# Kernel optimization log

Hardware: AMD Instinct MI355X
Metric: run time of the kernel (lower is better)

The kernel has to match this reference:

```python
import jax, jax.numpy as jnp
import numpy as np

TAU_MIN = 0.1
TAU_MAX = 5.0
EPS = 1e-8


def setup_inputs() -> dict:
    key = jax.random.key(0)
    ks = jax.random.split(key, 5)
    B, DK, NK, DV, H = 16384, 512, 4096, 512, 32
    return {
        "q": jax.random.normal(ks[0], (B, DK), dtype=jnp.float32),
        "keys": jax.random.normal(ks[1], (NK, DK), dtype=jnp.float32),
        "values": jax.random.normal(ks[2], (NK, DV), dtype=jnp.float32),
        "w1": jax.random.normal(ks[3], (H, 1), dtype=jnp.float32) * (6.0 / (H + 1)) ** 0.5,
        "b1": jnp.zeros((H,), dtype=jnp.float32),
        "w2": jax.random.normal(ks[4], (1, H), dtype=jnp.float32) * (6.0 / (H + 1)) ** 0.5,
        "b2": jnp.zeros((1,), dtype=jnp.float32),
    }


def reference(q, keys, values, w1, b1, w2, b2):
    d_k = q.shape[-1]
    n_keys = keys.shape[0]
    base_scale = d_k ** -0.5
    max_entropy = np.log(max(n_keys, 2)).astype(np.float32)

    # raw logits: (B, NK)
    raw_logits = jnp.matmul(q, keys.T)

    # entropy of base-scaled softmax
    p = jax.nn.softmax(raw_logits * base_scale, axis=-1)
    entropy = -jnp.sum(p * jnp.log(p + EPS), axis=-1, keepdims=True)  # (B,1)
    entropy = jnp.clip(entropy / (max_entropy + EPS), 0.0, 1.0)

    # entropy -> tau via tiny MLP (exact GELU, matching torch default)
    h = jax.nn.gelu(entropy @ w1.T + b1, approximate=False)  # (B,H)
    scale = jax.nn.sigmoid(h @ w2.T + b2)                    # (B,1)
    tau = TAU_MIN + (TAU_MAX - TAU_MIN) * scale

    # re-scaled softmax and final matmul
    scaled_logits = raw_logits * base_scale / (tau + EPS)
    attn_weights = jax.nn.softmax(scaled_logits, axis=-1)    # (B, NK)
    output = jnp.matmul(attn_weights, values)                # (B, DV)
    return output, attn_weights, entropy, tau
```

## Files before the change

### kernel.cpp

```cpp
#include <hip/hip_runtime.h>
#include <math.h>

#define B_ROWS 16384
#define DK     512
#define NK     4096
#define DV     512
#define H_MLP  32

typedef __attribute__((ext_vector_type(8))) short s16x8;
typedef __attribute__((ext_vector_type(4))) short s16x4;
typedef __attribute__((ext_vector_type(4))) float f32x4;

__device__ __forceinline__ short f2bf(float f) {
  unsigned u = __float_as_uint(f);
  u += 0x7fffu + ((u >> 16) & 1u);
  return (short)(u >> 16);
}

__device__ __forceinline__ void async_cp16(const short* g, short* l) {
  __builtin_amdgcn_global_load_lds(
      (const __attribute__((address_space(1))) unsigned int*)g,
      (__attribute__((address_space(3))) unsigned int*)l, 16, 0, 0);
}

__global__ __launch_bounds__(256) void cvt_bf16(const float* __restrict__ src,
                                                short* __restrict__ dst,
                                                long n, float scale) {
  long i = ((long)blockIdx.x * 256 + threadIdx.x) * 8;
  if (i >= n) return;
  float4 a = *(const float4*)(src + i);
  float4 b = *(const float4*)(src + i + 4);
  s16x8 o;
  o[0] = f2bf(a.x * scale); o[1] = f2bf(a.y * scale);
  o[2] = f2bf(a.z * scale); o[3] = f2bf(a.w * scale);
  o[4] = f2bf(b.x * scale); o[5] = f2bf(b.y * scale);
  o[6] = f2bf(b.z * scale); o[7] = f2bf(b.w * scale);
  *(s16x8*)(dst + i) = o;
}

__global__ __launch_bounds__(256) void transpose_v(const float* __restrict__ v,
                                                   short* __restrict__ vT) {
  __shared__ float tile[32][33];
  const int tx = threadIdx.x & 31;
  const int ty = threadIdx.x >> 5;
  const int k0 = blockIdx.x * 32;
  const int n0 = blockIdx.y * 32;
#pragma unroll
  for (int j = 0; j < 4; ++j)
    tile[ty + j * 8][tx] = v[(long)(k0 + ty + j * 8) * DV + n0 + tx];
  __syncthreads();
#pragma unroll
  for (int j = 0; j < 4; ++j)
    vT[(long)(n0 + ty + j * 8) * NK + k0 + tx] = f2bf(tile[tx][ty + j * 8]);
}

__device__ __forceinline__ void stage_f32_sw(const float* __restrict__ src, int ldk,
                                             int row0, int k0, short* lds, int tid) {
#pragma unroll
  for (int i = 0; i < 4; ++i) {
    int f   = i * 256 + tid;
    int row = f >> 3;
    int p   = f & 7;
    int c   = p ^ (row & 7);
    const float* gp = src + (long)(row0 + row) * ldk + k0 + c * 8;
    float4 a = *(const float4*)gp;
    float4 b = *(const float4*)(gp + 4);
    s16x8 o;
    o[0] = f2bf(a.x); o[1] = f2bf(a.y); o[2] = f2bf(a.z); o[3] = f2bf(a.w);
    o[4] = f2bf(b.x); o[5] = f2bf(b.y); o[6] = f2bf(b.z); o[7] = f2bf(b.w);
    *(s16x8*)(lds + row * 64 + p * 8) = o;
  }
}

__device__ __forceinline__ void stage_bf_async(const short* __restrict__ src, int ldk,
                                               int row0, int k0, short* lds,
                                               int w, int lane) {
  const int srow = lane >> 3;
  const int c    = (lane & 7) ^ srow;
  const short* g = src + (long)(row0 + w * 32 + srow) * ldk + k0 + c * 8;
  short* lb = lds + w * 2048;
#pragma unroll
  for (int i = 0; i < 4; ++i)
    async_cp16(g + (long)(i * 8) * ldk, lb + i * 512);
}

template <int AMODE, int BMODE>
__global__ __launch_bounds__(256) void gemm_nt(const void* __restrict__ Av,
                                               const void* __restrict__ Bv,
                                               float* __restrict__ C,
                                               int M, int N, int K, float alpha) {
  __shared__ short As[128 * 64];
  __shared__ short Bs[128 * 64];
  const int tid = threadIdx.x;

  const int nwg = gridDim.x * gridDim.y;
  const int bid = blockIdx.y * gridDim.x + blockIdx.x;
  const int per = nwg >> 3;
  const int swz = (bid & 7) * per + (bid >> 3);
  const int bx  = swz % gridDim.x;
  const int by  = swz / gridDim.x;

  const int rowBase = by * 128;
  const int colBase = bx * 128;
  const int w = tid >> 6, lane = tid & 63;
  const int waveM = w >> 1, waveN = w & 1;
  const int quad = lane >> 4, lr = lane & 15;
  const int sw = lr & 7;

  f32x4 acc[4][4];
#pragma unroll
  for (int i = 0; i < 4; ++i)
#pragma unroll
    for (int j = 0; j < 4; ++j)
      acc[i][j] = (f32x4){0.f, 0.f, 0.f, 0.f};

  for (int k0 = 0; k0 < K; k0 += 64) {
    __syncthreads();
    if constexpr (AMODE)
      stage_bf_async((const short*)Av, K, rowBase, k0, As, w, lane);
    else
      stage_f32_sw((const float*)Av, K, rowBase, k0, As, tid);
    if constexpr (BMODE)
      stage_bf_async((const short*)Bv, K, colBase, k0, Bs, w, lane);
    else
      stage_f32_sw((const float*)Bv, K, colBase, k0, Bs, tid);
    __syncthreads();
#pragma unroll
    for (int ks = 0; ks < 2; ++ks) {
      const int cpos = ((ks * 4 + quad) ^ sw) * 8;
      s16x8 a[4], b[4];
#pragma unroll
      for (int t = 0; t < 4; ++t) {
        a[t] = *(const s16x8*)(As + (waveM * 64 + t * 16 + lr) * 64 + cpos);
        b[t] = *(const s16x8*)(Bs + (waveN * 64 + t * 16 + lr) * 64 + cpos);
      }
#pragma unroll
      for (int mt = 0; mt < 4; ++mt)
#pragma unroll
        for (int nt = 0; nt < 4; ++nt)
          acc[mt][nt] = __builtin_amdgcn_mfma_f32_16x16x32_bf16(a[mt], b[nt], acc[mt][nt], 0, 0, 0);
    }
  }

#pragma unroll
  for (int mt = 0; mt < 4; ++mt)
#pragma unroll
    for (int nt = 0; nt < 4; ++nt) {
      int col = colBase + waveN * 64 + nt * 16 + lr;
#pragma unroll
      for (int r = 0; r < 4; ++r) {
        int row = rowBase + waveM * 64 + mt * 16 + quad * 4 + r;
        C[(long)row * N + col] = acc[mt][nt][r] * alpha;
      }
    }
}

__global__ __launch_bounds__(256) void entropy_softmax(
    float* __restrict__ l, short* __restrict__ attn_bf,
    float* __restrict__ ent_out, float* __restrict__ tau_out,
    const float* __restrict__ w1, const float* __restrict__ b1,
    const float* __restrict__ w2, const float* __restrict__ b2) {
  const int wid = threadIdx.x >> 6, lane = threadIdx.x & 63;
  const int row = blockIdx.x * 4 + wid;
  float4* lr = (float4*)(l + (long)row * NK);

  float4 v[16];
#pragma unroll
  for (int it = 0; it < 16; ++it) v[it] = lr[it * 64 + lane];

  float m = -3.4e38f;
#pragma unroll
  for (int it = 0; it < 16; ++it)
    m = fmaxf(m, fmaxf(fmaxf(v[it].x, v[it].y), fmaxf(v[it].z, v[it].w)));
#pragma unroll
  for (int off = 32; off >= 1; off >>= 1) m = fmaxf(m, __shfl_xor(m, off));

  float Z = 0.f, E1 = 0.f;
#pragma unroll
  for (int it = 0; it < 16; ++it) {
    float e0 = __expf(v[it].x - m), e1 = __expf(v[it].y - m);
    float e2 = __expf(v[it].z - m), e3 = __expf(v[it].w - m);
    Z  += (e0 + e1) + (e2 + e3);
    E1 += v[it].x * e0 + v[it].y * e1 + v[it].z * e2 + v[it].w * e3;
  }
#pragma unroll
  for (int off = 32; off >= 1; off >>= 1) {
    Z  += __shfl_xor(Z, off);
    E1 += __shfl_xor(E1, off);
  }

  float entropy = m + __logf(Z) - E1 / Z;
  float en = fminf(fmaxf(entropy / 8.3177662f, 0.f), 1.f);

  float hp = 0.f;
  if (lane < H_MLP) {
    float x = en * w1[lane] + b1[lane];
    float g = 0.5f * x * (1.f + erff(x * 0.70710678f));
    hp = g * w2[lane];
  }
#pragma unroll
  for (int off = 16; off >= 1; off >>= 1) hp += __shfl_xor(hp, off);
  hp = __shfl(hp, 0);

  float s    = 1.f / (1.f + __expf(-(hp + b2[0])));
  float tau  = 0.1f + 4.9f * s;
  float itau = 1.f / (tau + 1e-8f);
  if (lane == 0) { ent_out[row] = en; tau_out[row] = tau; }

  const float mi = m * itau;
  float Z2 = 0.f;
#pragma unroll
  for (int it = 0; it < 16; ++it) {
    v[it].x = __expf(fmaf(v[it].x, itau, -mi));
    v[it].y = __expf(fmaf(v[it].y, itau, -mi));
    v[it].z = __expf(fmaf(v[it].z, itau, -mi));
    v[it].w = __expf(fmaf(v[it].w, itau, -mi));
    Z2 += (v[it].x + v[it].y) + (v[it].z + v[it].w);
  }
#pragma unroll
  for (int off = 32; off >= 1; off >>= 1) Z2 += __shfl_xor(Z2, off);
  const float inv = 1.f / Z2;

  short* br = attn_bf ? attn_bf + (long)row * NK : nullptr;
#pragma unroll
  for (int it = 0; it < 16; ++it) {
    float4 p;
    p.x = v[it].x * inv; p.y = v[it].y * inv;
    p.z = v[it].z * inv; p.w = v[it].w * inv;
    lr[it * 64 + lane] = p;
    if (br) {
      s16x4 o;
      o.x = f2bf(p.x); o.y = f2bf(p.y); o.z = f2bf(p.z); o.w = f2bf(p.w);
      *(s16x4*)(br + (it * 64 + lane) * 4) = o;
    }
  }
}

extern "C" void kernel_launch(void* const* d_in, const int* in_sizes, int n_in,
                              void* d_out, int out_size, void* d_ws, size_t ws_size,
                              hipStream_t stream) {
  const float* q    = (const float*)d_in[0];
  const float* keys = (const float*)d_in[1];
  const float* vals = (const float*)d_in[2];
  const float* w1   = (const float*)d_in[3];
  const float* b1   = (const float*)d_in[4];
  const float* w2   = (const float*)d_in[5];
  const float* b2   = (const float*)d_in[6];

  float* out  = (float*)d_out;
  float* attn = out + (long)B_ROWS * DV;
  float* ent  = attn + (long)B_ROWS * NK;
  float* tau  = ent + B_ROWS;

  char* ws = (char*)d_ws;
  const size_t off_vT    = 0;
  const size_t off_keysb = off_vT + (size_t)DV * NK * 2;
  const size_t off_qb    = off_keysb + (size_t)NK * DK * 2;
  const size_t off_attnb = off_qb + (size_t)B_ROWS * DK * 2;
  const size_t need_mid  = off_attnb;
  const size_t need_full = off_attnb + (size_t)B_ROWS * NK * 2;

  short* vT    = (short*)(ws + off_vT);
  short* keysb = (short*)(ws + off_keysb);
  short* qb    = (short*)(ws + off_qb);
  short* attnb = (short*)(ws + off_attnb);

  const float base_scale = 0.044194173824159216f;

  transpose_v<<<dim3(NK / 32, DV / 32), 256, 0, stream>>>(vals, vT);

  if (ws_size >= need_mid) {
    cvt_bf16<<<(int)(((long)B_ROWS * DK) / 2048), 256, 0, stream>>>(
        q, qb, (long)B_ROWS * DK, base_scale);
    cvt_bf16<<<(int)(((long)NK * DK) / 2048), 256, 0, stream>>>(
        keys, keysb, (long)NK * DK, 1.0f);
    gemm_nt<1, 1><<<dim3(NK / 128, B_ROWS / 128), 256, 0, stream>>>(
        qb, keysb, attn, B_ROWS, NK, DK, 1.0f);
  } else {
    gemm_nt<0, 0><<<dim3(NK / 128, B_ROWS / 128), 256, 0, stream>>>(
        q, keys, attn, B_ROWS, NK, DK, base_scale);
  }

  const bool full = ws_size >= need_full;
  entropy_softmax<<<B_ROWS / 4, 256, 0, stream>>>(
      attn, full ? attnb : nullptr, ent, tau, w1, b1, w2, b2);

  if (full)
    gemm_nt<1, 1><<<dim3(DV / 128, B_ROWS / 128), 256, 0, stream>>>(
        attnb, vT, out, B_ROWS, DV, NK, 1.0f);
  else
    gemm_nt<0, 1><<<dim3(DV / 128, B_ROWS / 128), 256, 0, stream>>>(
        attn, vT, out, B_ROWS, DV, NK, 1.0f);
}
```

Before: 616.2 us.

## Add double-buffered async-LDS GEMM with larger tiles for both matmuls

Adds a templated GEMM that double-buffers the LDS tiles, issuing the async global-to-LDS copies for the next K step before computing the current one. Each K step then needs one barrier instead of two, and MFMA blocks are wrapped in raised wave priority. The QK^T GEMM moves to 256x256 tiles with 8 waves for more reuse per loaded tile, and the attn@V GEMM uses 128x128 tiles with the new pipeline. This doubles the LDS footprint per block, which may reduce how many blocks fit on a CU, and raises register pressure from the larger accumulator tile.

New measurement: 609.3 us. About the same (-1.1%).

```diff
diff --git a/kernel.cpp b/kernel.cpp
--- a/kernel.cpp
+++ b/kernel.cpp
@@ -72,15 +72,16 @@
   }
 }
 
+template <int RPW>
 __device__ __forceinline__ void stage_bf_async(const short* __restrict__ src, int ldk,
                                                int row0, int k0, short* lds,
                                                int w, int lane) {
   const int srow = lane >> 3;
   const int c    = (lane & 7) ^ srow;
-  const short* g = src + (long)(row0 + w * 32 + srow) * ldk + k0 + c * 8;
-  short* lb = lds + w * 2048;
-#pragma unroll
-  for (int i = 0; i < 4; ++i)
+  const short* g = src + (long)(row0 + w * RPW + srow) * ldk + k0 + c * 8;
+  short* lb = lds + w * RPW * 64;
+#pragma unroll
+  for (int i = 0; i < RPW / 8; ++i)
     async_cp16(g + (long)(i * 8) * ldk, lb + i * 512);
 }
 
@@ -117,11 +118,11 @@
   for (int k0 = 0; k0 < K; k0 += 64) {
     __syncthreads();
     if constexpr (AMODE)
-      stage_bf_async((const short*)Av, K, rowBase, k0, As, w, lane);
+      stage_bf_async<32>((const short*)Av, K, rowBase, k0, As, w, lane);
     else
       stage_f32_sw((const float*)Av, K, rowBase, k0, As, tid);
     if constexpr (BMODE)
-      stage_bf_async((const short*)Bv, K, colBase, k0, Bs, w, lane);
+      stage_bf_async<32>((const short*)Bv, K, colBase, k0, Bs, w, lane);
     else
       stage_f32_sw((const float*)Bv, K, colBase, k0, Bs, tid);
     __syncthreads();
@@ -150,6 +151,93 @@
 #pragma unroll
       for (int r = 0; r < 4; ++r) {
         int row = rowBase + waveM * 64 + mt * 16 + quad * 4 + r;
+        C[(long)row * N + col] = acc[mt][nt][r] * alpha;
+      }
+    }
+}
+
+template <int BM, int BN, int WM, int WN>
+__global__ __launch_bounds__(WM * WN * 64, 2) void gemm_nt_2ph(
+    const short* __restrict__ A, const short* __restrict__ B,
+    float* __restrict__ C, int M, int N, int K, float alpha) {
+  constexpr int NWAVE = WM * WN;
+  constexpr int MR = BM / WM / 16;
+  constexpr int NR = BN / WN / 16;
+  __shared__ short As[2 * BM * 64];
+  __shared__ short Bs[2 * BN * 64];
+
+  const int tid = threadIdx.x;
+  const int nwg = gridDim.x * gridDim.y;
+  const int bid = blockIdx.y * gridDim.x + blockIdx.x;
+  const int per = nwg >> 3;
+  const int swz = (bid & 7) * per + (bid >> 3);
+  const int bx  = swz % gridDim.x;
+  const int by  = swz / gridDim.x;
+
+  const int rowBase = by * BM;
+  const int colBase = bx * BN;
+  const int w = tid >> 6, lane = tid & 63;
+  const int waveM = w / WN, waveN = w % WN;
+  const int quad = lane >> 4, lr = lane & 15, sw = lr & 7;
+
+  f32x4 acc[MR][NR];
+#pragma unroll
+  for (int i = 0; i < MR; ++i)
+#pragma unroll
+    for (int j = 0; j < NR; ++j)
+      acc[i][j] = (f32x4){0.f, 0.f, 0.f, 0.f};
+
+  auto compute = [&](const short* Ab, const short* Bb) {
+#pragma unroll
+    for (int ks = 0; ks < 2; ++ks) {
+      const int cpos = ((ks * 4 + quad) ^ sw) * 8;
+      s16x8 a[MR], b[NR];
+#pragma unroll
+      for (int mt = 0; mt < MR; ++mt)
+        a[mt] = *(const s16x8*)(Ab + (waveM * (BM / WM) + mt * 16 + lr) * 64 + cpos);
+#pragma unroll
+      for (int nt = 0; nt < NR; ++nt)
+        b[nt] = *(const s16x8*)(Bb + (waveN * (BN / WN) + nt * 16 + lr) * 64 + cpos);
+      __builtin_amdgcn_s_setprio(1);
+#pragma unroll
+      for (int mt = 0; mt < MR; ++mt)
+#pragma unroll
+        for (int nt = 0; nt < NR; ++nt)
+          acc[mt][nt] = __builtin_amdgcn_mfma_f32_16x16x32_bf16(a[mt], b[nt], acc[mt][nt], 0, 0, 0);
+      __builtin_amdgcn_s_setprio(0);
+    }
+  };
+
+  const int NT = K >> 6;
+
+  stage_bf_async<BM / NWAVE>(A, K, rowBase, 0, As, w, lane);
+  stage_bf_async<BN / NWAVE>(B, K, colBase, 0, Bs, w, lane);
+  asm volatile("s_waitcnt vmcnt(0)" ::: "memory");
+  __builtin_amdgcn_s_barrier();
+  __builtin_amdgcn_sched_barrier(0);
+
+  int cur = 0;
+  for (int t = 0; t < NT - 1; ++t) {
+    const int nxt = cur ^ 1;
+    stage_bf_async<BM / NWAVE>(A, K, rowBase, (t + 1) * 64, As + nxt * BM * 64, w, lane);
+    stage_bf_async<BN / NWAVE>(B, K, colBase, (t + 1) * 64, Bs + nxt * BN * 64, w, lane);
+    __builtin_amdgcn_sched_barrier(0);
+    compute(As + cur * BM * 64, Bs + cur * BN * 64);
+    asm volatile("s_waitcnt vmcnt(0)" ::: "memory");
+    __builtin_amdgcn_s_barrier();
+    __builtin_amdgcn_sched_barrier(0);
+    cur = nxt;
+  }
+  compute(As + cur * BM * 64, Bs + cur * BN * 64);
+
+#pragma unroll
+  for (int mt = 0; mt < MR; ++mt)
+#pragma unroll
+    for (int nt = 0; nt < NR; ++nt) {
+      int col = colBase + waveN * (BN / WN) + nt * 16 + lr;
+#pragma unroll
+      for (int r = 0; r < 4; ++r) {
+        int row = rowBase + waveM * (BM / WM) + mt * 16 + quad * 4 + r;
         C[(long)row * N + col] = acc[mt][nt][r] * alpha;
       }
     }
@@ -274,7 +362,7 @@
         q, qb, (long)B_ROWS * DK, base_scale);
     cvt_bf16<<<(int)(((long)NK * DK) / 2048), 256, 0, stream>>>(
         keys, keysb, (long)NK * DK, 1.0f);
-    gemm_nt<1, 1><<<dim3(NK / 128, B_ROWS / 128), 256, 0, stream>>>(
+    gemm_nt_2ph<256, 256, 2, 4><<<dim3(NK / 256, B_ROWS / 256), 512, 0, stream>>>(
         qb, keysb, attn, B_ROWS, NK, DK, 1.0f);
   } else {
     gemm_nt<0, 0><<<dim3(NK / 128, B_ROWS / 128), 256, 0, stream>>>(
@@ -286,7 +374,7 @@
       attn, full ? attnb : nullptr, ent, tau, w1, b1, w2, b2);
 
   if (full)
-    gemm_nt<1, 1><<<dim3(DV / 128, B_ROWS / 128), 256, 0, stream>>>(
+    gemm_nt_2ph<128, 128, 2, 2><<<dim3(DV / 128, B_ROWS / 128), 256, 0, stream>>>(
         attnb, vT, out, B_ROWS, DV, NK, 1.0f);
   else
     gemm_nt<0, 1><<<dim3(DV / 128, B_ROWS / 128), 256, 0, stream>>>(
```
